# Kernel tuning notes

Measured on AMD Instinct MI355X. Metric: run time of the kernel, lower is better.

The kernel has to match this reference:

```python
import jax, jax.numpy as jnp
import numpy as np

N_NODES = 100000
N_EDGES = 1200000
D_IN = 64
D_HID = 64


def _gcn_layer(h_in, W, b, src, dst, norm, n_nodes):
    # h_in: [N, d_in]; W: [d_in, d_out]; norm: [E_total] symmetric deg norm
    h = h_in @ W                                  # [N, d_out]
    msg = h[src] * norm[:, None]                  # gather + scale, [E_total, d_out]
    agg = jax.ops.segment_sum(msg, dst, num_segments=n_nodes)  # scatter-add
    return agg + b


def _prelu(x, a):
    # per-channel PReLU: a broadcasts over nodes
    return jnp.where(x >= 0, x, a * x)


def setup_inputs() -> dict:
    key = jax.random.key(0)
    ks = jax.random.split(key, 8)
    x = jax.random.normal(ks[0], (N_NODES, D_IN), dtype=jnp.float32)
    edge_index = jax.random.randint(ks[1], (2, N_EDGES), 0, N_NODES, dtype=jnp.int64)
    # Glorot-ish weights, PyG GCNConv defaults: weight + bias; PReLU init slope 0.25
    W1 = jax.random.normal(ks[2], (D_IN, D_HID), dtype=jnp.float32) / np.sqrt(D_IN)
    b1 = jnp.zeros((D_HID,), dtype=jnp.float32)
    a1 = jnp.full((D_HID,), 0.25, dtype=jnp.float32)
    W2 = jax.random.normal(ks[3], (D_HID, D_HID), dtype=jnp.float32) / np.sqrt(D_HID)
    b2 = jnp.zeros((D_HID,), dtype=jnp.float32)
    a2 = jnp.full((D_HID,), 0.25, dtype=jnp.float32)
    return {"x": x, "edge_index": edge_index, "W1": W1, "b1": b1, "a1": a1,
            "W2": W2, "b2": b2, "a2": a2}


def reference(x, edge_index, W1, b1, a1, W2, b2, a2):
    n = x.shape[0]
    # add self-loops (GCNConv default add_self_loops=True)
    loops = jnp.arange(n, dtype=edge_index.dtype)
    src = jnp.concatenate([edge_index[0], loops])
    dst = jnp.concatenate([edge_index[1], loops])
    # symmetric normalization: deg computed on destination with unit edge weights
    deg = jax.ops.segment_sum(jnp.ones_like(src, dtype=x.dtype), dst, num_segments=n)
    dinv = jnp.where(deg > 0, jax.lax.rsqrt(deg), 0.0)
    norm = dinv[src] * dinv[dst]                  # [E + N]

    h = _gcn_layer(x, W1, b1, src, dst, norm, n)
    h = _prelu(h, a1)
    h = _gcn_layer(h, W2, b2, src, dst, norm, n)
    h = _prelu(h, a2)
    return h
```

## Files before the change

kernel.cpp:

```cpp
#include <hip/hip_runtime.h>
#include <hip/hip_bf16.h>
#include <hip/hip_fp16.h>

#define D 64
#define GXN 16
#define NB 256
#define BSHIFT 8
#define CAP 3584
#define CHUNK 2048
#define AGN 32
#define BFSTRIDE 16


__global__ void __launch_bounds__(256, 4)
k_bin_gemm(const int* __restrict__ src, const int* __restrict__ dst,
           unsigned* __restrict__ records, int* __restrict__ bucket_fill,
           int E, int nbin,
           const float* __restrict__ X, const float* __restrict__ W,
           __half* __restrict__ H, int n, int ntiles, int gemmb) {
    __shared__ int cnt[512];
    __shared__ int gbase[512];
    const int t = threadIdx.x;

    if ((int)blockIdx.x < nbin) {
        cnt[t] = 0; cnt[t + 256] = 0;
        __syncthreads();

        const int base_e = blockIdx.x * CHUNK;
        unsigned rec[8];
        unsigned br[8];
#pragma unroll
        for (int i = 0; i < 8; ++i) {
            int e = base_e + i * 256 + t;
            if (e < E) {
                int s = src[e], d = dst[e];
                int bk = d >> BSHIFT;
                rec[i] = ((unsigned)s << BSHIFT) | (unsigned)(d & (NB - 1));
                int rank = atomicAdd(&cnt[bk], 1);
                br[i] = ((unsigned)bk << 16) | (unsigned)rank;
            } else {
                br[i] = 0xFFFFFFFFu;
            }
        }
        __syncthreads();
#pragma unroll
        for (int rep = 0; rep < 2; ++rep) {
            int bk = t + rep * 256;
            if (cnt[bk] > 0)
                gbase[bk] = atomicAdd(&bucket_fill[bk * BFSTRIDE], cnt[bk]);
        }
        __syncthreads();
#pragma unroll
        for (int i = 0; i < 8; ++i) {
            if (br[i] != 0xFFFFFFFFu) {
                int bk = br[i] >> 16;
                int idx = gbase[bk] + (int)(br[i] & 0xFFFF);
                if (idx < CAP)
                    records[(size_t)bk * CAP + idx] = rec[i];
            }
        }
    } else {
        const int lane = t & 63;
        const int wv   = t >> 6;
        float wreg[64];
#pragma unroll
        for (int k = 0; k < D; ++k) wreg[k] = W[k * D + lane];

        const int bid = blockIdx.x - nbin;
        for (int tile = bid; tile < ntiles; tile += gemmb) {
            const int nb4 = tile * GXN + wv * 4;
            const int ln  = nb4 + (lane >> 4);
            float4 xv = make_float4(0.f, 0.f, 0.f, 0.f);
            if (ln < n)
                xv = *reinterpret_cast<const float4*>(X + (size_t)ln * D + (lane & 15) * 4);
            float xc[4] = {xv.x, xv.y, xv.z, xv.w};
#pragma unroll
            for (int g = 0; g < 4; ++g) {
                const int node = nb4 + g;
                if (node >= n) break;
                float acc = 0.f;
#pragma unroll
                for (int k = 0; k < D; ++k) {
                    float xk = __uint_as_float(__builtin_amdgcn_readlane(
                        __float_as_uint(xc[k & 3]), g * 16 + (k >> 2)));
                    acc = fmaf(xk, wreg[k], acc);
                }
                H[(size_t)node * D + lane] = __float2half_rn(acc);
            }
        }
    }
}


__global__ void k_csr(const unsigned* __restrict__ records,
                      const int* __restrict__ bucket_fill,
                      int* __restrict__ rowptr, float* __restrict__ dinv,
                      int* __restrict__ csr_src, __half* __restrict__ H,
                      int n, int E) {
    __shared__ int bscan[256];
    __shared__ int binc[512];
    __shared__ int cnt[NB];
    __shared__ int excl[NB];
    __shared__ float ddi[NB];
    __shared__ int stage[CAP];

    const int t = threadIdx.x;
    const int b = blockIdx.x;
    const int nbuckets = gridDim.x;

    int s0 = (2 * t     < nbuckets) ? bucket_fill[(2 * t)     * BFSTRIDE] : 0;
    int s1 = (2 * t + 1 < nbuckets) ? bucket_fill[(2 * t + 1) * BFSTRIDE] : 0;
    bscan[t] = s0 + s1;
    __syncthreads();
    for (int off = 1; off < 256; off <<= 1) {
        int val = bscan[t];
        if (t >= off) val += bscan[t - off];
        __syncthreads();
        bscan[t] = val;
        __syncthreads();
    }
    {
        int ep = bscan[t] - (s0 + s1);
        binc[2 * t]     = ep + s0;
        binc[2 * t + 1] = ep + s0 + s1;
    }
    __syncthreads();
    const int base  = (b == 0) ? 0 : binc[b - 1];
    const int cnt_e = binc[b] - base;
    if (b == nbuckets - 1 && t == 0) rowptr[n] = binc[nbuckets - 1];

    cnt[t] = 0;
    __syncthreads();
    for (int i = t; i < cnt_e; i += 256)
        atomicAdd(&cnt[records[(size_t)b * CAP + i] & (NB - 1)], 1);
    __syncthreads();

    const int c0 = cnt[t];
    bscan[t] = c0;
    __syncthreads();
    for (int off = 1; off < 256; off <<= 1) {
        int val = bscan[t];
        if (t >= off) val += bscan[t - off];
        __syncthreads();
        bscan[t] = val;
        __syncthreads();
    }
    excl[t] = bscan[t] - c0;
    {
        int node = b * NB + t;
        float di = rsqrtf((float)(c0 + 1));
        ddi[t] = di;
        if (node < n) {
            rowptr[node] = base + excl[t];
            dinv[node]   = di;
        }
        cnt[t] = 0;
    }
    __syncthreads();

    for (int i = t; i < cnt_e; i += 256) {
        unsigned r = records[(size_t)b * CAP + i];
        int d8 = r & (NB - 1);
        int rank = atomicAdd(&cnt[d8], 1);
        stage[excl[d8] + rank] = (int)(r >> BSHIFT);
    }
    __syncthreads();

    for (int i = t; i < cnt_e; i += 256)
        csr_src[base + i] = stage[i];

#pragma unroll
    for (int r = 0; r < (NB * 8) / 256; ++r) {
        int idx = r * 256 + t;
        int nl = idx >> 3;
        int node = b * NB + nl;
        if (node < n) {
            int part = (idx & 7) * 8;
            uint4 g = *reinterpret_cast<uint4*>(H + (size_t)node * D + part);
            __half2* p = reinterpret_cast<__half2*>(&g);
            float s = ddi[nl];
#pragma unroll
            for (int i = 0; i < 4; ++i) {
                float2 f = __half22float2(p[i]);
                p[i] = __floats2half2_rn(f.x * s, f.y * s);
            }
            *reinterpret_cast<uint4*>(H + (size_t)node * D + part) = g;
        }
    }
}

__device__ __forceinline__ void edge_accum(const __half* __restrict__ Hn,
                                           const int* __restrict__ csr_src,
                                           int beg, int end, int part, float acc[8]) {
    int i0 = 0, i1 = 0, i2 = 0, i3 = 0;
    if (beg     < end) i0 = csr_src[beg];
    if (beg + 1 < end) i1 = csr_src[beg + 1];
    if (beg + 2 < end) i2 = csr_src[beg + 2];
    if (beg + 3 < end) i3 = csr_src[beg + 3];
    int k = beg;
    while (k < end) {
        int s0 = i0, s1 = i1, s2 = i2, s3 = i3;
        float w1 = (k + 1 < end) ? 1.f : 0.f;
        float w2 = (k + 2 < end) ? 1.f : 0.f;
        float w3 = (k + 3 < end) ? 1.f : 0.f;
        int kn = k + 4;
        i0 = (kn     < end) ? csr_src[kn]     : 0;
        i1 = (kn + 1 < end) ? csr_src[kn + 1] : 0;
        i2 = (kn + 2 < end) ? csr_src[kn + 2] : 0;
        i3 = (kn + 3 < end) ? csr_src[kn + 3] : 0;
        uint4 g0 = *reinterpret_cast<const uint4*>(Hn + (size_t)s0 * D + part);
        uint4 g1 = *reinterpret_cast<const uint4*>(Hn + (size_t)s1 * D + part);
        uint4 g2 = *reinterpret_cast<const uint4*>(Hn + (size_t)s2 * D + part);
        uint4 g3 = *reinterpret_cast<const uint4*>(Hn + (size_t)s3 * D + part);
        const __half2* p0 = reinterpret_cast<const __half2*>(&g0);
        const __half2* p1 = reinterpret_cast<const __half2*>(&g1);
        const __half2* p2 = reinterpret_cast<const __half2*>(&g2);
        const __half2* p3 = reinterpret_cast<const __half2*>(&g3);
#pragma unroll
        for (int i = 0; i < 4; ++i) {
            float2 f0 = __half22float2(p0[i]);
            float2 f1 = __half22float2(p1[i]);
            float2 f2 = __half22float2(p2[i]);
            float2 f3 = __half22float2(p3[i]);
            acc[2 * i + 0] += f0.x + w1 * f1.x + w2 * f2.x + w3 * f3.x;
            acc[2 * i + 1] += f0.y + w1 * f1.y + w2 * f2.y + w3 * f3.y;
        }
        k = kn;
    }
}


__global__ void k_agg_gemm(const __half* __restrict__ Hn1,
                           const int* __restrict__ rowptr,
                           const int* __restrict__ csr_src,
                           const float* __restrict__ dinv,
                           const float* __restrict__ b1, const float* __restrict__ a1,
                           const float* __restrict__ W2,
                           __half* __restrict__ Hn2, int n) {
    __shared__ float W2l[D * D];
    __shared__ float Yl[AGN][68];

    const int t = threadIdx.x;
    for (int i = t; i < (D * D) / 4; i += 256)
        *reinterpret_cast<float4*>(W2l + i * 4) = *reinterpret_cast<const float4*>(W2 + i * 4);

    const int nl   = t >> 3;
    const int part = (t & 7) * 8;
    const int node = blockIdx.x * AGN + nl;

    float di = 0.f;
    if (node < n) {
        di = dinv[node];
        float acc[8];
        {
            uint4 g = *reinterpret_cast<const uint4*>(Hn1 + (size_t)node * D + part);
            const __half2* p = reinterpret_cast<const __half2*>(&g);
#pragma unroll
            for (int i = 0; i < 4; ++i) {
                float2 f = __half22float2(p[i]);
                acc[2 * i + 0] = f.x;
                acc[2 * i + 1] = f.y;
            }
        }
        edge_accum(Hn1, csr_src, rowptr[node], rowptr[node + 1], part, acc);

        const float4 b0 = *reinterpret_cast<const float4*>(b1 + part);
        const float4 b4 = *reinterpret_cast<const float4*>(b1 + part + 4);
        const float4 a0 = *reinterpret_cast<const float4*>(a1 + part);
        const float4 a4 = *reinterpret_cast<const float4*>(a1 + part + 4);
        float y0 = acc[0] * di + b0.x, y1 = acc[1] * di + b0.y;
        float y2 = acc[2] * di + b0.z, y3 = acc[3] * di + b0.w;
        float y4 = acc[4] * di + b4.x, y5 = acc[5] * di + b4.y;
        float y6 = acc[6] * di + b4.z, y7 = acc[7] * di + b4.w;
        Yl[nl][part + 0] = (y0 >= 0.f) ? y0 : a0.x * y0;
        Yl[nl][part + 1] = (y1 >= 0.f) ? y1 : a0.y * y1;
        Yl[nl][part + 2] = (y2 >= 0.f) ? y2 : a0.z * y2;
        Yl[nl][part + 3] = (y3 >= 0.f) ? y3 : a0.w * y3;
        Yl[nl][part + 4] = (y4 >= 0.f) ? y4 : a4.x * y4;
        Yl[nl][part + 5] = (y5 >= 0.f) ? y5 : a4.y * y5;
        Yl[nl][part + 6] = (y6 >= 0.f) ? y6 : a4.z * y6;
        Yl[nl][part + 7] = (y7 >= 0.f) ? y7 : a4.w * y7;
    }
    __syncthreads();

    if (node >= n) return;
    float o[8];
#pragma unroll
    for (int i = 0; i < 8; ++i) o[i] = 0.f;
#pragma unroll 8
    for (int k = 0; k < D; ++k) {
        float yk = Yl[nl][k];
        float4 w0 = *reinterpret_cast<const float4*>(W2l + k * D + part);
        float4 w1 = *reinterpret_cast<const float4*>(W2l + k * D + part + 4);
        o[0] += yk * w0.x; o[1] += yk * w0.y; o[2] += yk * w0.z; o[3] += yk * w0.w;
        o[4] += yk * w1.x; o[5] += yk * w1.y; o[6] += yk * w1.z; o[7] += yk * w1.w;
    }
    __half2 h0 = __floats2half2_rn(o[0] * di, o[1] * di);
    __half2 h1 = __floats2half2_rn(o[2] * di, o[3] * di);
    __half2 h2 = __floats2half2_rn(o[4] * di, o[5] * di);
    __half2 h3 = __floats2half2_rn(o[6] * di, o[7] * di);
    uint4 pack;
    pack.x = *reinterpret_cast<unsigned int*>(&h0);
    pack.y = *reinterpret_cast<unsigned int*>(&h1);
    pack.z = *reinterpret_cast<unsigned int*>(&h2);
    pack.w = *reinterpret_cast<unsigned int*>(&h3);
    *reinterpret_cast<uint4*>(Hn2 + (size_t)node * D + part) = pack;
}


__global__ void k_aggregate(const __half* __restrict__ Hn,
                            const int* __restrict__ rowptr,
                            const int* __restrict__ csr_src,
                            const float* __restrict__ dinv,
                            const float* __restrict__ b, const float* __restrict__ a,
                            float* __restrict__ out, int n) {
    int t = blockIdx.x * blockDim.x + threadIdx.x;
    int node = t >> 3;
    if (node >= n) return;
    int part = (t & 7) * 8;

    float di = dinv[node];
    float acc[8];
    {
        uint4 g = *reinterpret_cast<const uint4*>(Hn + (size_t)node * D + part);
        const __half2* p = reinterpret_cast<const __half2*>(&g);
#pragma unroll
        for (int i = 0; i < 4; ++i) {
            float2 f = __half22float2(p[i]);
            acc[2 * i + 0] = f.x;
            acc[2 * i + 1] = f.y;
        }
    }
    edge_accum(Hn, csr_src, rowptr[node], rowptr[node + 1], part, acc);

    const float4 b0 = *reinterpret_cast<const float4*>(b + part);
    const float4 b4 = *reinterpret_cast<const float4*>(b + part + 4);
    const float4 a0 = *reinterpret_cast<const float4*>(a + part);
    const float4 a4 = *reinterpret_cast<const float4*>(a + part + 4);
    float4 r0, r1;
    r0.x = acc[0] * di + b0.x; r0.y = acc[1] * di + b0.y;
    r0.z = acc[2] * di + b0.z; r0.w = acc[3] * di + b0.w;
    r1.x = acc[4] * di + b4.x; r1.y = acc[5] * di + b4.y;
    r1.z = acc[6] * di + b4.z; r1.w = acc[7] * di + b4.w;
    r0.x = (r0.x >= 0.f) ? r0.x : a0.x * r0.x;
    r0.y = (r0.y >= 0.f) ? r0.y : a0.y * r0.y;
    r0.z = (r0.z >= 0.f) ? r0.z : a0.z * r0.z;
    r0.w = (r0.w >= 0.f) ? r0.w : a0.w * r0.w;
    r1.x = (r1.x >= 0.f) ? r1.x : a4.x * r1.x;
    r1.y = (r1.y >= 0.f) ? r1.y : a4.y * r1.y;
    r1.z = (r1.z >= 0.f) ? r1.z : a4.z * r1.z;
    r1.w = (r1.w >= 0.f) ? r1.w : a4.w * r1.w;
    float* o = out + (size_t)node * D + part;
    *reinterpret_cast<float4*>(o) = r0;
    *reinterpret_cast<float4*>(o + 4) = r1;
}

extern "C" void kernel_launch(void* const* d_in, const int* in_sizes, int n_in,
                              void* d_out, int out_size, void* d_ws, size_t ws_size,
                              hipStream_t stream) {
    const float* x  = (const float*)d_in[0];
    const int*   ei = (const int*)  d_in[1];
    const float* W1 = (const float*)d_in[2];
    const float* b1 = (const float*)d_in[3];
    const float* a1 = (const float*)d_in[4];
    const float* W2 = (const float*)d_in[5];
    const float* b2 = (const float*)d_in[6];
    const float* a2 = (const float*)d_in[7];
    float* out = (float*)d_out;

    const int n   = in_sizes[0] / D;
    const int E   = in_sizes[1] / 2;
    const int n64 = n * D;

    const int* src = ei;
    const int* dst = ei + E;

    const int nbuckets = (n + NB - 1) >> BSHIFT;

    int*      bucket_fill = (int*)d_ws;
    unsigned* records     = (unsigned*)(bucket_fill + 512 * BFSTRIDE);
    int*      rowptr      = (int*)(records + (size_t)nbuckets * CAP);
    float*    dinv        = (float*)(rowptr + ((n + 257) & ~255));
    int*      csr_src     = (int*)(dinv + ((n + 256) & ~255));
    __half*   Hn1         = (__half*)(csr_src + ((E + 255) & ~255));
    __half*   Hn2         = Hn1 + (((size_t)n64 + 256) & ~(size_t)255);

    const int B = 256;
    const int nbin   = (E + CHUNK - 1) / CHUNK;
    const int gemmb  = 1024;
    const int ntiles = (n + GXN - 1) / GXN;

    hipMemsetAsync(bucket_fill, 0, 512 * BFSTRIDE * sizeof(int), stream);

    k_bin_gemm<<<nbin + gemmb, B, 0, stream>>>(src, dst, records, bucket_fill, E, nbin,
                                               x, W1, Hn1, n, ntiles, gemmb);
    k_csr<<<nbuckets, B, 0, stream>>>(records, bucket_fill, rowptr, dinv, csr_src,
                                      Hn1, n, E);
    k_agg_gemm<<<(n + AGN - 1) / AGN, B, 0, stream>>>(Hn1, rowptr, csr_src, dinv,
                                                      b1, a1, W2, Hn2, n);
    k_aggregate<<<(n * 8 + B - 1) / B, B, 0, stream>>>(Hn2, rowptr, csr_src, dinv,
                                                       b2, a2, out, n);
}
```

Baseline: 215.5 us.

## Hold W2 columns in registers and broadcast activations via readlane in fused agg-GEMM

Removes the 16KB shared-memory copy of W2 in the fused aggregation+GEMM kernel. Each lane now keeps one column of W2 in 64 registers, and the node's hidden row is broadcast through readlane from a float4 shared-memory load. Freeing the shared memory and adding launch bounds is meant to raise occupancy for the latency-bound gather phase. The cost is heavy register pressure, scalar 2-byte output stores instead of packed 16-byte stores, and 64 readlanes per node.

```diff
diff --git a/kernel.cpp b/kernel.cpp
--- a/kernel.cpp
+++ b/kernel.cpp
@@ -230,27 +230,29 @@
 }
 
 
-__global__ void k_agg_gemm(const __half* __restrict__ Hn1,
-                           const int* __restrict__ rowptr,
-                           const int* __restrict__ csr_src,
-                           const float* __restrict__ dinv,
-                           const float* __restrict__ b1, const float* __restrict__ a1,
-                           const float* __restrict__ W2,
-                           __half* __restrict__ Hn2, int n) {
-    __shared__ float W2l[D * D];
+__global__ void __launch_bounds__(256, 4)
+k_agg_gemm(const __half* __restrict__ Hn1,
+           const int* __restrict__ rowptr,
+           const int* __restrict__ csr_src,
+           const float* __restrict__ dinv,
+           const float* __restrict__ b1, const float* __restrict__ a1,
+           const float* __restrict__ W2,
+           __half* __restrict__ Hn2, int n) {
     __shared__ float Yl[AGN][68];
+    __shared__ float ddi[AGN];
 
     const int t = threadIdx.x;
-    for (int i = t; i < (D * D) / 4; i += 256)
-        *reinterpret_cast<float4*>(W2l + i * 4) = *reinterpret_cast<const float4*>(W2 + i * 4);
-
     const int nl   = t >> 3;
     const int part = (t & 7) * 8;
     const int node = blockIdx.x * AGN + nl;
 
-    float di = 0.f;
+    if (t < AGN) {
+        int nn = blockIdx.x * AGN + t;
+        ddi[t] = (nn < n) ? dinv[nn] : 0.f;
+    }
+
     if (node < n) {
-        di = dinv[node];
+        float di = dinv[node];
         float acc[8];
         {
             uint4 g = *reinterpret_cast<const uint4*>(Hn1 + (size_t)node * D + part);
@@ -283,28 +285,31 @@
     }
     __syncthreads();
 
-    if (node >= n) return;
-    float o[8];
-#pragma unroll
-    for (int i = 0; i < 8; ++i) o[i] = 0.f;
-#pragma unroll 8
-    for (int k = 0; k < D; ++k) {
-        float yk = Yl[nl][k];
-        float4 w0 = *reinterpret_cast<const float4*>(W2l + k * D + part);
-        float4 w1 = *reinterpret_cast<const float4*>(W2l + k * D + part + 4);
-        o[0] += yk * w0.x; o[1] += yk * w0.y; o[2] += yk * w0.z; o[3] += yk * w0.w;
-        o[4] += yk * w1.x; o[5] += yk * w1.y; o[6] += yk * w1.z; o[7] += yk * w1.w;
-    }
-    __half2 h0 = __floats2half2_rn(o[0] * di, o[1] * di);
-    __half2 h1 = __floats2half2_rn(o[2] * di, o[3] * di);
-    __half2 h2 = __floats2half2_rn(o[4] * di, o[5] * di);
-    __half2 h3 = __floats2half2_rn(o[6] * di, o[7] * di);
-    uint4 pack;
-    pack.x = *reinterpret_cast<unsigned int*>(&h0);
-    pack.y = *reinterpret_cast<unsigned int*>(&h1);
-    pack.z = *reinterpret_cast<unsigned int*>(&h2);
-    pack.w = *reinterpret_cast<unsigned int*>(&h3);
-    *reinterpret_cast<uint4*>(Hn2 + (size_t)node * D + part) = pack;
+    const int lane = t & 63;
+    const int wv   = t >> 6;
+    float w2reg[64];
+#pragma unroll
+    for (int k = 0; k < D; ++k) w2reg[k] = W2[k * D + lane];
+
+#pragma unroll
+    for (int rep = 0; rep < 2; ++rep) {
+        const int nb4 = wv * 4 + rep * 16;
+        float4 yv = *reinterpret_cast<float4*>(&Yl[nb4 + (lane >> 4)][(lane & 15) * 4]);
+        float xc[4] = {yv.x, yv.y, yv.z, yv.w};
+#pragma unroll
+        for (int g = 0; g < 4; ++g) {
+            const int nd = blockIdx.x * AGN + nb4 + g;
+            if (nd >= n) break;
+            float o = 0.f;
+#pragma unroll
+            for (int k = 0; k < D; ++k) {
+                float xk = __uint_as_float(__builtin_amdgcn_readlane(
+                    __float_as_uint(xc[k & 3]), g * 16 + (k >> 2)));
+                o = fmaf(xk, w2reg[k], o);
+            }
+            Hn2[(size_t)nd * D + lane] = __float2half_rn(o * ddi[nb4 + g]);
+        }
+    }
 }
 
 
```

Result: slower. 226.1 us (+4.9%).
